# Optimization experiments

Hardware: AMD Instinct MI355X
Metric: run time of the kernel (lower is better)

## Reference

```python
import jax, jax.numpy as jnp
import numpy as np

N, C, D, H, OUT = 8192, 128, 512, 512, 2
OBS_SCALE = 10.0
WHEELBASE = 2.96
DT = 0.1
DT_DISCRE = 100
C_R = 0.0
C_A = 0.0


def setup_inputs() -> dict:
    key = jax.random.key(0)
    ks = jax.random.split(key, 8)
    def w(k, shape, fan_in):
        return (jax.random.normal(k, shape, jnp.float32) / np.float32(np.sqrt(fan_in)))
    return {
        "obs": jax.random.normal(ks[0], (N, C), jnp.float32),
        "Wq": w(ks[1], (C, D), C), "bq": jnp.zeros((D,), jnp.float32),
        "Wk": w(ks[2], (C, D), C), "bk": jnp.zeros((D,), jnp.float32),
        "Wv": w(ks[3], (C, D), C), "bv": jnp.zeros((D,), jnp.float32),
        "W1": w(ks[4], (D, H), D), "b1": jnp.zeros((H,), jnp.float32),
        "g1": jnp.ones((H,), jnp.float32), "beta1": jnp.zeros((H,), jnp.float32),
        "W2": w(ks[5], (H, OUT), H), "b2": jnp.zeros((OUT,), jnp.float32),
    }


def reference(obs, Wq, bq, Wk, bk, Wv, bv, W1, b1, g1, beta1, W2, b2):
    # ---- self-attention GNN over agents (obs.unsqueeze(0) -> [1, N, C]) ----
    x = obs[None]                                   # [1, n, c]
    q = x @ Wq + bq                                 # [1, n, d]
    k = x @ Wk + bk
    v = x @ Wv + bv
    scores = jnp.einsum("bnd,bmd->bnm", q, k) / np.float32(np.sqrt(D))
    attn = jax.nn.softmax(scores, axis=-1)          # [1, n, n]
    out = jnp.einsum("bnm,bmd->bnd", attn, v)       # [1, n, d]
    # ---- trajectory prediction MLP: Linear -> LayerNorm -> ReLU -> Linear ----
    h = out @ W1 + b1                               # [1, n, h]
    mu = h.mean(axis=-1, keepdims=True)
    var = ((h - mu) ** 2).mean(axis=-1, keepdims=True)
    h = (h - mu) * jax.lax.rsqrt(var + 1e-5) * g1 + beta1
    h = jax.nn.relu(h)
    pred_action = h @ W2 + b2                       # [1, n, 2]

    throttle = pred_action[0, :, 0]                 # [n]
    delta = pred_action[0, :, 1]                    # [n]

    # ---- kinematic bicycle model, 100 serial sub-steps, vectorized over n ----
    x0 = obs[:, 0] * OBS_SCALE
    y0 = obs[:, 1] * OBS_SCALE
    yaw0 = obs[:, 4] * OBS_SCALE
    v0 = jnp.sqrt((obs[:, 2] * OBS_SCALE) ** 2 + (obs[:, 3] * OBS_SCALE) ** 2)
    dt_s = np.float32(DT / DT_DISCRE)

    def step(carry, _):
        xx, yy, yw, vv = carry
        f_load = vv * (vv * C_A + C_R)
        vv = vv + (throttle - f_load) * dt_s        # velocity updated first (as in source)
        xx = xx + vv * jnp.cos(yw) * dt_s
        yy = yy + vv * jnp.sin(yw) * dt_s
        yw = yw + vv * jnp.tan(delta) * (1.0 / WHEELBASE) * dt_s
        yw = jnp.arctan2(jnp.sin(yw), jnp.cos(yw))  # wrap to (-pi, pi]
        return (xx, yy, yw, vv), None

    (xf, yf, ywf, vf), _ = jax.lax.scan(step, (x0, y0, yaw0, v0), None, length=DT_DISCRE)

    pred_state = jnp.stack(
        [xf / OBS_SCALE,
         yf / OBS_SCALE,
         vf * jnp.cos(ywf) / OBS_SCALE,
         vf * jnp.sin(ywf) / OBS_SCALE,
         ywf / OBS_SCALE],
        axis=-1)                                    # [n, 5]
    return pred_state
```

## Files before the change

### kernel.cpp

```cpp
#include <hip/hip_runtime.h>
#include <stdint.h>


typedef __attribute__((ext_vector_type(4))) float f32x4;

__device__ __forceinline__ float readlane_f(float v, int lane) {
  return __uint_as_float(__builtin_amdgcn_readlane(__float_as_uint(v), lane));
}

typedef __attribute__((address_space(3))) uint32_t lds_u32;
typedef const __attribute__((address_space(1))) uint32_t glb_u32;
__device__ __forceinline__ void gload16(const void* g, void* l) {
  __builtin_amdgcn_global_load_lds((glb_u32*)g, (lds_u32*)l, 16, 0, 0);
}

__global__ __launch_bounds__(256) void qkv_f32(
    const float* __restrict__ obs,
    const float* __restrict__ Wq, const float* __restrict__ bq,
    const float* __restrict__ Wk, const float* __restrict__ bk,
    const float* __restrict__ Wv, const float* __restrict__ bv,
    float* __restrict__ Qf, float* __restrict__ Kf, float* __restrict__ Vf)
{
  __shared__ float smA[32][128];
  __shared__ float smB[64][128];
  const int t  = threadIdx.x;
  const int cb = blockIdx.x;
  const int rb = blockIdx.y;
  const float* W; const float* bias; float* Op;
  if (cb < 4)      { W = Wq; bias = bq; Op = Qf; }
  else if (cb < 8) { W = Wk; bias = bk; Op = Kf; }
  else             { W = Wv; bias = bv; Op = Vf; }
  const int col0 = (cb & 3) * 128;

  {
    const float4* src = (const float4*)(obs + (size_t)rb * (32 * 128));
    float4* dst = (float4*)&smA[0][0];
#pragma unroll
    for (int i = 0; i < 4; ++i) dst[i * 256 + t] = src[i * 256 + t];
  }

  const int tr = t >> 5, tc = t & 31;
  float acc[4][4] = {};
#pragma unroll 1
  for (int kc = 0; kc < 2; ++kc) {
    __syncthreads();
#pragma unroll
    for (int i = 0; i < 8; ++i) {
      int id = i * 256 + t;
      int kr = id >> 5, c4 = id & 31;
      *(float4*)&smB[kr][c4 * 4] =
          *(const float4*)(W + (size_t)(kc * 64 + kr) * 512 + col0 + c4 * 4);
    }
    __syncthreads();
#pragma unroll 4
    for (int k2 = 0; k2 < 64; ++k2) {
      float4 b = *(const float4*)&smB[k2][tc * 4];
      float a0 = smA[tr * 4 + 0][kc * 64 + k2];
      float a1 = smA[tr * 4 + 1][kc * 64 + k2];
      float a2 = smA[tr * 4 + 2][kc * 64 + k2];
      float a3 = smA[tr * 4 + 3][kc * 64 + k2];
#pragma unroll
      for (int j = 0; j < 4; ++j) {
        acc[0][j] += a0 * b[j];
        acc[1][j] += a1 * b[j];
        acc[2][j] += a2 * b[j];
        acc[3][j] += a3 * b[j];
      }
    }
  }

  float4 bb = *(const float4*)(bias + col0 + tc * 4);
  const int r0 = rb * 32 + tr * 4;
#pragma unroll
  for (int ii = 0; ii < 4; ++ii) {
    float4 o;
#pragma unroll
    for (int j = 0; j < 4; ++j) o[j] = acc[ii][j] + bb[j];
    *(float4*)(Op + (size_t)(r0 + ii) * 512 + col0 + tc * 4) = o;
  }
}

#define FLASH_NSLOTS 1024

__global__ __launch_bounds__(512, 2) void flash_f32(
    const float* __restrict__ Q, const float* __restrict__ K,
    const float* __restrict__ V, float* __restrict__ Out)
{
  __shared__ __align__(16) char lds[163840];
  float* Qlds = (float*)lds;
  char*  bufb = lds + 65536;
  const int t  = threadIdx.x;
  const int tx = t & 63;
  const int w  = t >> 6;
  const int qrow0 = blockIdx.x * 32;
  const int r0 = qrow0 + w * 4;
  const float sc = 0.04419417382415922f;

  auto stage = [&](int S, int bidx) {
    if (S >= FLASH_NSLOTS) S = FLASH_NSLOTS - 1;
    char* lb = bufb + (bidx << 15);
    const int kt = S >> 5, sub = S & 31;
    if (sub < 16) {
      const int key_in = tx >> 3;
      const int csw = ((tx & 7) ^ key_in) << 4;
      const char* gb = (const char*)K + ((size_t)kt * 256) * 2048
                     + (size_t)sub * 128 + csw;
#pragma unroll
      for (int c = 0; c < 4; ++c)
        gload16(gb + (size_t)((c * 8 + w) * 8 + key_in) * 2048,
                lb + ((c * 8 + w) << 10));
    } else {
      const char* gb = (const char*)V
                     + ((size_t)(kt * 256 + (sub - 16) * 16)) * 2048 + tx * 16;
#pragma unroll
      for (int c = 0; c < 4; ++c)
        gload16(gb + ((c * 8 + w) << 10), lb + ((c * 8 + w) << 10));
    }
  };

  {
    const char* gq = (const char*)Q + (size_t)qrow0 * 2048 + tx * 16;
#pragma unroll
    for (int c = 0; c < 8; ++c)
      gload16(gq + ((c * 8 + w) << 10), lds + ((c * 8 + w) << 10));
  }
  stage(0, 0);
  stage(1, 1);
  asm volatile("s_waitcnt vmcnt(4)" ::: "memory");
  __builtin_amdgcn_s_barrier();

  float O[4][8];
#pragma unroll
  for (int i = 0; i < 4; ++i)
#pragma unroll
    for (int n = 0; n < 8; ++n) O[i][n] = 0.f;
  float m[4], l[4];
#pragma unroll
  for (int i = 0; i < 4; ++i) { m[i] = -1e30f; l[i] = 0.f; }

  int S = 0, bc = 0, bi = 2;
  const int qbase = (w * 4) * 512 + (tx & 31);
  const int kswz = (tx & 7) << 4;

#pragma unroll 1
  for (int kt = 0; kt < 32; ++kt) {
    float p[4][4];
#pragma unroll
    for (int i = 0; i < 4; ++i)
#pragma unroll
      for (int j = 0; j < 4; ++j) p[i][j] = 0.f;

#pragma unroll 1
    for (int s = 0; s < 16; ++s) {
      stage(S + 2, bi);
      const char* kb = bufb + (bc << 15);
      float qs[4];
#pragma unroll
      for (int i = 0; i < 4; ++i) qs[i] = Qlds[qbase + i * 512 + s * 32];
#pragma unroll
      for (int u8 = 0; u8 < 8; ++u8) {
        f32x4 kv[4];
#pragma unroll
        for (int j = 0; j < 4; ++j)
          kv[j] = *(const f32x4*)(kb + ((j * 64 + tx) << 7) + ((u8 * 16) ^ kswz));
#pragma unroll
        for (int e = 0; e < 4; ++e) {
          float q0 = readlane_f(qs[0], u8 * 4 + e);
          float q1 = readlane_f(qs[1], u8 * 4 + e);
          float q2 = readlane_f(qs[2], u8 * 4 + e);
          float q3 = readlane_f(qs[3], u8 * 4 + e);
#pragma unroll
          for (int j = 0; j < 4; ++j) {
            p[0][j] = fmaf(q0, kv[j][e], p[0][j]);
            p[1][j] = fmaf(q1, kv[j][e], p[1][j]);
            p[2][j] = fmaf(q2, kv[j][e], p[2][j]);
            p[3][j] = fmaf(q3, kv[j][e], p[3][j]);
          }
        }
      }
      asm volatile("s_waitcnt vmcnt(4)" ::: "memory");
      __builtin_amdgcn_s_barrier();
      ++S; bc = (bc == 2) ? 0 : bc + 1; bi = (bi == 2) ? 0 : bi + 1;
    }

#pragma unroll
    for (int i = 0; i < 4; ++i) {
      float rmax = -1e30f;
#pragma unroll
      for (int j = 0; j < 4; ++j) { p[i][j] *= sc; rmax = fmaxf(rmax, p[i][j]); }
#pragma unroll
      for (int o = 1; o < 64; o <<= 1) rmax = fmaxf(rmax, __shfl_xor(rmax, o));
      float mn = fmaxf(m[i], rmax);
      float corr = __expf(m[i] - mn);
      m[i] = mn;
      float ps = 0.f;
#pragma unroll
      for (int j = 0; j < 4; ++j) { float e = __expf(p[i][j] - mn); p[i][j] = e; ps += e; }
#pragma unroll
      for (int o = 1; o < 64; o <<= 1) ps += __shfl_xor(ps, o);
      l[i] = l[i] * corr + ps;
#pragma unroll
      for (int n = 0; n < 8; ++n) O[i][n] *= corr;
    }

#pragma unroll
    for (int j = 0; j < 4; ++j) {
      float pj0 = p[0][j], pj1 = p[1][j], pj2 = p[2][j], pj3 = p[3][j];
#pragma unroll 1
      for (int v2 = 0; v2 < 4; ++v2) {
        stage(S + 2, bi);
        const char* vbuf = bufb + (bc << 15) + (tx << 4);
        const int bl = v2 * 16;
#pragma unroll
        for (int kk = 0; kk < 16; ++kk) {
          float pv0 = readlane_f(pj0, bl + kk);
          float pv1 = readlane_f(pj1, bl + kk);
          float pv2 = readlane_f(pj2, bl + kk);
          float pv3 = readlane_f(pj3, bl + kk);
          f32x4 va = *(const f32x4*)(vbuf + (kk << 11));
          f32x4 vb = *(const f32x4*)(vbuf + (kk << 11) + 1024);
#pragma unroll
          for (int e = 0; e < 4; ++e) {
            O[0][e] = fmaf(pv0, va[e], O[0][e]);
            O[1][e] = fmaf(pv1, va[e], O[1][e]);
            O[2][e] = fmaf(pv2, va[e], O[2][e]);
            O[3][e] = fmaf(pv3, va[e], O[3][e]);
            O[0][4 + e] = fmaf(pv0, vb[e], O[0][4 + e]);
            O[1][4 + e] = fmaf(pv1, vb[e], O[1][4 + e]);
            O[2][4 + e] = fmaf(pv2, vb[e], O[2][4 + e]);
            O[3][4 + e] = fmaf(pv3, vb[e], O[3][4 + e]);
          }
        }
        asm volatile("s_waitcnt vmcnt(4)" ::: "memory");
        __builtin_amdgcn_s_barrier();
        ++S; bc = (bc == 2) ? 0 : bc + 1; bi = (bi == 2) ? 0 : bi + 1;
      }
    }
  }

#pragma unroll
  for (int i = 0; i < 4; ++i) {
    float inv = 1.0f / l[i];
    float4 oa, ob;
#pragma unroll
    for (int e = 0; e < 4; ++e) { oa[e] = O[i][e] * inv; ob[e] = O[i][4 + e] * inv; }
    *(float4*)(Out + (size_t)(r0 + i) * 512 + tx * 4) = oa;
    *(float4*)(Out + (size_t)(r0 + i) * 512 + 256 + tx * 4) = ob;
  }
}

__global__ __launch_bounds__(256) void mlp1_kernel(
    const float* __restrict__ X, const float* __restrict__ W1,
    const float* __restrict__ b1, float* __restrict__ Ho)
{
  __shared__ float smA[32][64];
  __shared__ float smB[64][128];
  const int t = threadIdx.x;
  const int cb = blockIdx.x;
  const int rb = blockIdx.y;
  const int col0 = cb * 128;
  const int tr = t >> 5, tc = t & 31;
  float acc[4][4] = {};
#pragma unroll 1
  for (int kc = 0; kc < 8; ++kc) {
    __syncthreads();
#pragma unroll
    for (int i = 0; i < 2; ++i) {
      int id = i * 256 + t;
      int r = id >> 4, c4 = id & 15;
      *(float4*)&smA[r][c4 * 4] =
          *(const float4*)(X + (size_t)(rb * 32 + r) * 512 + kc * 64 + c4 * 4);
    }
#pragma unroll
    for (int i = 0; i < 8; ++i) {
      int id = i * 256 + t;
      int kr = id >> 5, c4 = id & 31;
      *(float4*)&smB[kr][c4 * 4] =
          *(const float4*)(W1 + (size_t)(kc * 64 + kr) * 512 + col0 + c4 * 4);
    }
    __syncthreads();
#pragma unroll 4
    for (int k2 = 0; k2 < 64; ++k2) {
      float4 b = *(const float4*)&smB[k2][tc * 4];
      float a0 = smA[tr * 4 + 0][k2];
      float a1 = smA[tr * 4 + 1][k2];
      float a2 = smA[tr * 4 + 2][k2];
      float a3 = smA[tr * 4 + 3][k2];
#pragma unroll
      for (int j = 0; j < 4; ++j) {
        acc[0][j] += a0 * b[j];
        acc[1][j] += a1 * b[j];
        acc[2][j] += a2 * b[j];
        acc[3][j] += a3 * b[j];
      }
    }
  }
  const int r0 = rb * 32 + tr * 4;
  float4 bb = *(const float4*)(b1 + col0 + tc * 4);
#pragma unroll
  for (int ii = 0; ii < 4; ++ii) {
    float4 o;
#pragma unroll
    for (int j = 0; j < 4; ++j) o[j] = acc[ii][j] + bb[j];
    *(float4*)(Ho + (size_t)(r0 + ii) * 512 + col0 + tc * 4) = o;
  }
}

__global__ __launch_bounds__(256) void act_kernel(
    const float* __restrict__ H, const float* __restrict__ g1,
    const float* __restrict__ be1, const float* __restrict__ W2,
    const float* __restrict__ b2, float* __restrict__ act)
{
  const int lane = threadIdx.x & 63;
  const int w = threadIdx.x >> 6;
  const int row = blockIdx.x * 4 + w;
  const float* h = H + (size_t)row * 512;
  float x[8];
  *(float4*)&x[0] = *(const float4*)(h + lane * 8);
  *(float4*)&x[4] = *(const float4*)(h + lane * 8 + 4);
  float s = 0.f;
#pragma unroll
  for (int j = 0; j < 8; ++j) s += x[j];
#pragma unroll
  for (int o = 1; o < 64; o <<= 1) s += __shfl_xor(s, o);
  const float mu = s * (1.0f / 512.0f);
  float vs = 0.f;
#pragma unroll
  for (int j = 0; j < 8; ++j) { float d = x[j] - mu; vs += d * d; }
#pragma unroll
  for (int o = 1; o < 64; o <<= 1) vs += __shfl_xor(vs, o);
  const float rs = 1.0f / sqrtf(vs * (1.0f / 512.0f) + 1e-5f);
  float at = 0.f, ad = 0.f;
#pragma unroll
  for (int j = 0; j < 8; ++j) {
    int c = lane * 8 + j;
    float xn = (x[j] - mu) * rs * g1[c] + be1[c];
    xn = fmaxf(xn, 0.0f);
    at += xn * W2[2 * c];
    ad += xn * W2[2 * c + 1];
  }
#pragma unroll
  for (int o = 1; o < 64; o <<= 1) { at += __shfl_xor(at, o); ad += __shfl_xor(ad, o); }
  if (lane == 0) {
    act[row * 2 + 0] = at + b2[0];
    act[row * 2 + 1] = ad + b2[1];
  }
}

__global__ __launch_bounds__(256) void physics_kernel(
    const float* __restrict__ obs, const float* __restrict__ act,
    float* __restrict__ out)
{
  const int row = blockIdx.x * 256 + threadIdx.x;
  const float* o = obs + (size_t)row * 128;
  float xx = o[0] * 10.0f;
  float yy = o[1] * 10.0f;
  float vx = o[2] * 10.0f;
  float vy = o[3] * 10.0f;
  float yw = o[4] * 10.0f;
  float vv = sqrtf(vx * vx + vy * vy);
  const float th = act[row * 2 + 0];
  const float de = act[row * 2 + 1];
  const float dt_s = 0.001f;
  const float inv_wb = (float)(1.0 / 2.96);
  const float td = tanf(de);
#pragma unroll 1
  for (int i = 0; i < 100; ++i) {
    vv = vv + th * dt_s;
    float s1 = sinf(yw), c1 = cosf(yw);
    xx = xx + vv * c1 * dt_s;
    yy = yy + vv * s1 * dt_s;
    yw = yw + ((vv * td) * inv_wb) * dt_s;
    yw = atan2f(sinf(yw), cosf(yw));
  }
  float cf = cosf(yw), sf = sinf(yw);
  out[row * 5 + 0] = xx * 0.1f;
  out[row * 5 + 1] = yy * 0.1f;
  out[row * 5 + 2] = vv * cf * 0.1f;
  out[row * 5 + 3] = vv * sf * 0.1f;
  out[row * 5 + 4] = yw * 0.1f;
}

extern "C" void kernel_launch(void* const* d_in, const int* in_sizes, int n_in,
                              void* d_out, int out_size, void* d_ws, size_t ws_size,
                              hipStream_t stream) {
  const float* obs = (const float*)d_in[0];
  const float* Wq  = (const float*)d_in[1];
  const float* bq  = (const float*)d_in[2];
  const float* Wk  = (const float*)d_in[3];
  const float* bk  = (const float*)d_in[4];
  const float* Wv  = (const float*)d_in[5];
  const float* bv  = (const float*)d_in[6];
  const float* W1  = (const float*)d_in[7];
  const float* b1  = (const float*)d_in[8];
  const float* g1  = (const float*)d_in[9];
  const float* be1 = (const float*)d_in[10];
  const float* W2  = (const float*)d_in[11];
  const float* b2  = (const float*)d_in[12];

  char* ws = (char*)d_ws;
  float* Qf  = (float*)(ws);
  float* Kf  = (float*)(ws + (size_t)(16 << 20));
  float* Vf  = (float*)(ws + (size_t)(32 << 20));
  float* Aout= (float*)(ws + (size_t)(48 << 20));
  float* Ho  = (float*)(ws);
  float* Act = (float*)(ws + (size_t)(16 << 20));
  float* out = (float*)d_out;

  qkv_f32<<<dim3(12, 256), 256, 0, stream>>>(obs, Wq, bq, Wk, bk, Wv, bv, Qf, Kf, Vf);
  flash_f32<<<dim3(256), 512, 0, stream>>>(Qf, Kf, Vf, Aout);
  mlp1_kernel<<<dim3(4, 256), 256, 0, stream>>>(Aout, W1, b1, Ho);
  act_kernel<<<dim3(2048), 256, 0, stream>>>(Ho, g1, be1, W2, b2, Act);
  physics_kernel<<<dim3(32), 256, 0, stream>>>(obs, Act, out);
}
```

Measured before the change: 2.482 ms.

## Read V directly from global memory in flash kernel, stage only K through LDS

The flash attention kernel stops staging V tiles into LDS. The P·V loop now loads V rows straight from global memory into registers, and the LDS pipeline slots only cover K, so the slot count is halved. This removes the per-V-chunk barriers and the LDS traffic for V. In exchange, every wave re-reads V from global memory or L2, with no asynchronous prefetch, so load latency is exposed inside the FMA loop.

Result: faster. 2.425 ms (-2.3%).

```diff
diff --git a/kernel.cpp b/kernel.cpp
--- a/kernel.cpp
+++ b/kernel.cpp
@@ -80,7 +80,7 @@
   }
 }
 
-#define FLASH_NSLOTS 1024
+#define FLASH_NSLOTS 512
 
 __global__ __launch_bounds__(512, 2) void flash_f32(
     const float* __restrict__ Q, const float* __restrict__ K,
@@ -99,23 +99,15 @@
   auto stage = [&](int S, int bidx) {
     if (S >= FLASH_NSLOTS) S = FLASH_NSLOTS - 1;
     char* lb = bufb + (bidx << 15);
-    const int kt = S >> 5, sub = S & 31;
-    if (sub < 16) {
-      const int key_in = tx >> 3;
-      const int csw = ((tx & 7) ^ key_in) << 4;
-      const char* gb = (const char*)K + ((size_t)kt * 256) * 2048
-                     + (size_t)sub * 128 + csw;
-#pragma unroll
-      for (int c = 0; c < 4; ++c)
-        gload16(gb + (size_t)((c * 8 + w) * 8 + key_in) * 2048,
-                lb + ((c * 8 + w) << 10));
-    } else {
-      const char* gb = (const char*)V
-                     + ((size_t)(kt * 256 + (sub - 16) * 16)) * 2048 + tx * 16;
-#pragma unroll
-      for (int c = 0; c < 4; ++c)
-        gload16(gb + ((c * 8 + w) << 10), lb + ((c * 8 + w) << 10));
-    }
+    const int kt = S >> 4, sub = S & 15;
+    const int key_in = tx >> 3;
+    const int csw = ((tx & 7) ^ key_in) << 4;
+    const char* gb = (const char*)K + ((size_t)kt * 256) * 2048
+                   + (size_t)sub * 128 + csw;
+#pragma unroll
+    for (int c = 0; c < 4; ++c)
+      gload16(gb + (size_t)((c * 8 + w) * 8 + key_in) * 2048,
+              lb + ((c * 8 + w) << 10));
   };
 
   {
@@ -207,18 +199,24 @@
     for (int j = 0; j < 4; ++j) {
       float pj0 = p[0][j], pj1 = p[1][j], pj2 = p[2][j], pj3 = p[3][j];
 #pragma unroll 1
-      for (int v2 = 0; v2 < 4; ++v2) {
-        stage(S + 2, bi);
-        const char* vbuf = bufb + (bc << 15) + (tx << 4);
-        const int bl = v2 * 16;
-#pragma unroll
-        for (int kk = 0; kk < 16; ++kk) {
-          float pv0 = readlane_f(pj0, bl + kk);
-          float pv1 = readlane_f(pj1, bl + kk);
-          float pv2 = readlane_f(pj2, bl + kk);
-          float pv3 = readlane_f(pj3, bl + kk);
-          f32x4 va = *(const f32x4*)(vbuf + (kk << 11));
-          f32x4 vb = *(const f32x4*)(vbuf + (kk << 11) + 1024);
+      for (int kc = 0; kc < 16; ++kc) {
+        const float* vbase = V + (size_t)(kt * 256 + j * 64 + kc * 4) * 512 + tx * 4;
+        f32x4 va0 = *(const f32x4*)(vbase);
+        f32x4 vb0 = *(const f32x4*)(vbase + 256);
+        f32x4 va1 = *(const f32x4*)(vbase + 512);
+        f32x4 vb1 = *(const f32x4*)(vbase + 768);
+        f32x4 va2 = *(const f32x4*)(vbase + 1024);
+        f32x4 vb2 = *(const f32x4*)(vbase + 1280);
+        f32x4 va3 = *(const f32x4*)(vbase + 1536);
+        f32x4 vb3 = *(const f32x4*)(vbase + 1792);
+#pragma unroll
+        for (int kk = 0; kk < 4; ++kk) {
+          const f32x4 va = (kk == 0) ? va0 : (kk == 1) ? va1 : (kk == 2) ? va2 : va3;
+          const f32x4 vb = (kk == 0) ? vb0 : (kk == 1) ? vb1 : (kk == 2) ? vb2 : vb3;
+          float pv0 = readlane_f(pj0, kc * 4 + kk);
+          float pv1 = readlane_f(pj1, kc * 4 + kk);
+          float pv2 = readlane_f(pj2, kc * 4 + kk);
+          float pv3 = readlane_f(pj3, kc * 4 + kk);
 #pragma unroll
           for (int e = 0; e < 4; ++e) {
             O[0][e] = fmaf(pv0, va[e], O[0][e]);
@@ -231,9 +229,6 @@
             O[3][4 + e] = fmaf(pv3, vb[e], O[3][4 + e]);
           }
         }
-        asm volatile("s_waitcnt vmcnt(4)" ::: "memory");
-        __builtin_amdgcn_s_barrier();
-        ++S; bc = (bc == 2) ? 0 : bc + 1; bi = (bi == 2) ? 0 : bi + 1;
       }
     }
   }
```
